# Performance work log

Measured on AMD Instinct MI355X. Metric: run time of the kernel, lower is better.

The kernel has to match this reference:

```python
import jax, jax.numpy as jnp
import numpy as np

B, C, H, W = 8, 2, 512, 512  # features hard-coded to 2 by Conv3x3(2,1)
N_ATTN = 6  # 3 ResidualAttentionUnits x 2 AttentionConv each
HALF = C // 2


def _conv1x1(x, w, b):
    # x: [B,C,H,W], w: [O,C], b: [O]
    return jnp.einsum('bchw,oc->bohw', x, w) + b[None, :, None, None]


def _unfold3(x):
    # x: [B,C,H+2,W+2] -> [B,C,H,W,3,3] (height-window, width-window), matching
    # torch unfold(2,3,1).unfold(3,3,1)
    Hh = x.shape[2] - 2
    Ww = x.shape[3] - 2
    return jnp.stack(
        [jnp.stack([x[:, :, i:i + Hh, j:j + Ww] for j in range(3)], axis=-1)
         for i in range(3)], axis=-2)


def _attn_conv(x, wq, bq, wk, bk, wv, bv, rh, rw):
    # Local 3x3 window self-attention (AttentionConv, groups=1).
    b_, c_, h_, w_ = x.shape
    xp = jnp.pad(x, ((0, 0), (0, 0), (1, 1), (1, 1)))  # zero pad=1
    q = _conv1x1(x, wq, bq)                 # [B,Co,H,W]
    k = _unfold3(_conv1x1(xp, wk, bk))      # [B,Co,H,W,3,3]
    v = _unfold3(_conv1x1(xp, wv, bv))
    co = q.shape[1]
    half = co // 2
    # rh, rw: [half,3]; rel_h broadcast over kh, rel_w over kw
    k = jnp.concatenate([
        k[:, :half] + rh[None, :, None, None, :, None],
        k[:, half:] + rw[None, :, None, None, None, :]], axis=1)
    k = k.reshape(b_, co, h_, w_, 9)
    v = v.reshape(b_, co, h_, w_, 9)
    attn = jax.nn.softmax(q[..., None] * k, axis=-1)  # softmax over 9 window positions
    return jnp.einsum('bchwk,bchwk->bchw', attn, v)


def _rau(x, p, u):
    # ResidualAttentionUnit: relu -> atten1 -> relu -> atten2 -> +x
    wq, bq, wk, bk, wv, bv, rh, rw = p
    i, j = 2 * u, 2 * u + 1
    h = jax.nn.relu(x)
    h = _attn_conv(h, wq[i], bq[i], wk[i], bk[i], wv[i], bv[i], rh[i], rw[i])
    h = jax.nn.relu(h)
    h = _attn_conv(h, wq[j], bq[j], wk[j], bk[j], wv[j], bv[j], rh[j], rw[j])
    return h + x


def _up2_bilinear_ac(x):
    # bilinear, scale_factor=2, align_corners=True
    b_, c_, h_, w_ = x.shape
    ho, wo = 2 * h_, 2 * w_
    ys = jnp.linspace(0.0, h_ - 1.0, ho)
    xs = jnp.linspace(0.0, w_ - 1.0, wo)
    y0 = jnp.floor(ys).astype(jnp.int32)
    x0 = jnp.floor(xs).astype(jnp.int32)
    y1 = jnp.clip(y0 + 1, 0, h_ - 1)
    x1 = jnp.clip(x0 + 1, 0, w_ - 1)
    wy = (ys - y0)[None, None, :, None]
    wx = (xs - x0)[None, None, None, :]
    r0 = x[:, :, y0, :]
    r1 = x[:, :, y1, :]
    v00 = r0[:, :, :, x0]
    v01 = r0[:, :, :, x1]
    v10 = r1[:, :, :, x0]
    v11 = r1[:, :, :, x1]
    return (v00 * (1 - wy) * (1 - wx) + v01 * (1 - wy) * wx
            + v10 * wy * (1 - wx) + v11 * wy * wx)


def _forward(input_1, input_2, wq, bq, wk, bk, wv, bv, rh, rw, conv_w, conv_b):
    p = (wq, bq, wk, bk, wv, bv, rh, rw)
    out = _rau(input_1, p, 0) + _rau(input_2, p, 1)
    out = _rau(out, p, 2)
    xp = jnp.pad(out, ((0, 0), (0, 0), (1, 1), (1, 1)), mode='reflect')
    out = jax.lax.conv_general_dilated(
        xp, conv_w, (1, 1), 'VALID',
        dimension_numbers=('NCHW', 'OIHW', 'NCHW')) + conv_b[None, :, None, None]
    out = jax.nn.sigmoid(out)
    return out, _up2_bilinear_ac(out)


def setup_inputs() -> dict:
    key = jax.random.key(0)
    ks = jax.random.split(key, 12)
    return {
        'input_1': jax.random.normal(ks[0], (B, C, H, W), jnp.float32),
        'input_2': jax.random.normal(ks[1], (B, C, H, W), jnp.float32),
        # stacked params for the 6 AttentionConv modules (all bias=True)
        'wq': jax.random.normal(ks[2], (N_ATTN, C, C), jnp.float32) * 0.5,
        'bq': jax.random.normal(ks[3], (N_ATTN, C), jnp.float32) * 0.1,
        'wk': jax.random.normal(ks[4], (N_ATTN, C, C), jnp.float32) * 0.5,
        'bk': jax.random.normal(ks[5], (N_ATTN, C), jnp.float32) * 0.1,
        'wv': jax.random.normal(ks[6], (N_ATTN, C, C), jnp.float32) * 0.5,
        'bv': jax.random.normal(ks[7], (N_ATTN, C), jnp.float32) * 0.1,
        'rh': jax.random.normal(ks[8], (N_ATTN, HALF, 3), jnp.float32),
        'rw': jax.random.normal(ks[9], (N_ATTN, HALF, 3), jnp.float32),
        # Conv3x3(2,1): reflection-pad + 3x3 conv
        'conv_w': jax.random.normal(ks[10], (1, 2, 3, 3), jnp.float32) * 0.2,
        'conv_b': jax.random.normal(ks[11], (1,), jnp.float32) * 0.1,
    }


def reference(input_1, input_2, wq, bq, wk, bk, wv, bv, rh, rw, conv_w, conv_b):
    return _forward(input_1, input_2, wq, bq, wk, bk, wv, bv, rh, rw, conv_w, conv_b)
```

## Files before the change

kernel.cpp:

```cpp
#include <hip/hip_runtime.h>

#if __has_builtin(__builtin_amdgcn_exp2f)
#define EXP2F(x) __builtin_amdgcn_exp2f(x)
#else
#define EXP2F(x) exp2f(x)
#endif

typedef float v2f __attribute__((ext_vector_type(2)));

constexpr int B = 8, H = 512, W = 512;
constexpr int PLANE = H * W;
constexpr int BSTRIDE = 2 * PLANE;
constexpr int NPIX = B * PLANE;
constexpr int PPITCH = 520;
constexpr int PXOFF  = 4;
constexpr int PPLANE = H * PPITCH;
constexpr int PBUF   = 16 * PPLANE;
constexpr float LOG2E = 1.4426950408889634f;

__device__ __forceinline__ float reluf(float v) { return v > 0.f ? v : 0.f; }
__device__ __forceinline__ float frcp(float v) { return __builtin_amdgcn_rcpf(v); }
__device__ __forceinline__ v2f vfma(v2f a, v2f b, v2f c) { return __builtin_elementwise_fma(a, b, c); }
__device__ __forceinline__ v2f vmax2(v2f a, v2f b) { return __builtin_elementwise_max(a, b); }
__device__ __forceinline__ v2f bc(float x) { v2f r; r.x = x; r.y = x; return r; }

__device__ __forceinline__ unsigned swz8(unsigned bid, unsigned nwg)
{
    return (bid & 7u) * (nwg >> 3) + (bid >> 3);
}

struct AttnW {
    v2f wq0, wq1, bq;
    v2f wk0, wk1;
    v2f biasK[3];
    float rwL[3];
    v2f wv0, wv1, bv;
};

__device__ __forceinline__ AttnW load_w(
    const float* wq, const float* bq, const float* wk, const float* bk,
    const float* wv, const float* bv, const float* rh, const float* rw, int i)
{
    AttnW P;
    P.wq0.x = wq[4*i];   P.wq0.y = wq[4*i+2];
    P.wq1.x = wq[4*i+1]; P.wq1.y = wq[4*i+3];
    P.bq.x  = bq[2*i];   P.bq.y  = bq[2*i+1];
    P.wk0.x = wk[4*i]   * LOG2E; P.wk0.y = wk[4*i+2] * LOG2E;
    P.wk1.x = wk[4*i+1] * LOG2E; P.wk1.y = wk[4*i+3] * LOG2E;
    float bk1L = bk[2*i+1] * LOG2E;
#pragma unroll
    for (int r = 0; r < 3; ++r) {
        P.biasK[r].x = (bk[2*i] + rh[3*i+r]) * LOG2E;
        P.biasK[r].y = bk1L;
    }
#pragma unroll
    for (int d = 0; d < 3; ++d) P.rwL[d] = rw[3*i+d] * LOG2E;
    P.wv0.x = wv[4*i];   P.wv0.y = wv[4*i+2];
    P.wv1.x = wv[4*i+1]; P.wv1.y = wv[4*i+3];
    P.bv.x  = bv[2*i];   P.bv.y  = bv[2*i+1];
    return P;
}

__device__ __forceinline__ void attn_strip(
    const v2f (&t)[3][6], const AttnW& P, v2f (&o)[4])
{
    v2f kk[3][6], vv[3][6];
#pragma unroll
    for (int r = 0; r < 3; ++r)
#pragma unroll
        for (int c = 0; c < 6; ++c) {
            v2f u0 = bc(t[r][c].x), u1 = bc(t[r][c].y);
            kk[r][c] = vfma(P.wk0, u0, vfma(P.wk1, u1, P.biasK[r]));
            vv[r][c] = vfma(P.wv0, u0, vfma(P.wv1, u1, P.bv));
        }
#pragma unroll
    for (int px = 0; px < 4; ++px) {
        v2f q = vfma(P.wq0, bc(t[1][px+1].x), vfma(P.wq1, bc(t[1][px+1].y), P.bq));
        v2f addv[3];
#pragma unroll
        for (int d = 0; d < 3; ++d) { addv[d].x = 0.f; addv[d].y = q.y * P.rwL[d]; }
        v2f s[9];
#pragma unroll
        for (int r = 0; r < 3; ++r)
#pragma unroll
            for (int d = 0; d < 3; ++d)
                s[r*3+d] = vfma(q, kk[r][px+d], addv[d]);
        v2f m = vmax2(vmax2(vmax2(vmax2(s[0], s[1]), vmax2(s[2], s[3])),
                            vmax2(vmax2(s[4], s[5]), vmax2(s[6], s[7]))), s[8]);
        v2f sum = bc(0.f), acc = bc(0.f);
#pragma unroll
        for (int r = 0; r < 3; ++r)
#pragma unroll
            for (int d = 0; d < 3; ++d) {
                v2f dd = s[r*3+d] - m;
                v2f e; e.x = EXP2F(dd.x); e.y = EXP2F(dd.y);
                sum += e;
                acc = vfma(e, vv[r][px+d], acc);
            }
        v2f rs; rs.x = frcp(sum.x); rs.y = frcp(sum.y);
        o[px] = acc * rs;
    }
}

__device__ __forceinline__ void write_pads(float* outp, int b2, int y, int x0)
{
    float4 z = make_float4(0.f, 0.f, 0.f, 0.f);
    if (x0 == 0) {
        int pb = b2 * PPLANE + y * PPITCH;
        *reinterpret_cast<float4*>(outp + pb)          = z;
        *reinterpret_cast<float4*>(outp + pb + PPLANE) = z;
    } else if (x0 == W - 4) {
        int pb = b2 * PPLANE + y * PPITCH + PXOFF + W;
        *reinterpret_cast<float4*>(outp + pb)          = z;
        *reinterpret_cast<float4*>(outp + pb + PPLANE) = z;
    }
}


__device__ __forceinline__ void load_t_unpadded(
    unsigned s, const float* __restrict__ x, v2f (&t)[3][6])
{
    int x0 = (s & 127) * 4;
    int y  = (s >> 7) & 511;
    int b  = s >> 16;

    const float* xb = x + b * BSTRIDE;
    bool rowv[3] = { y > 0, true, y < H - 1 };
    int  yr[3]   = { y > 0 ? y - 1 : 0, y, y < H - 1 ? y + 1 : H - 1 };
    bool lv   = x0 > 0;
    bool rvld = x0 < W - 4;
    int  xl = lv ? x0 - 1 : 0;
    int  xr = rvld ? x0 + 4 : W - 1;

#pragma unroll
    for (int r = 0; r < 3; ++r) {
        const float* p0 = xb + yr[r] * W;
        const float* p1 = p0 + PLANE;
        float4 a0 = *reinterpret_cast<const float4*>(p0 + x0);
        float4 a1 = *reinterpret_cast<const float4*>(p1 + x0);
        float u0[6] = { p0[xl], a0.x, a0.y, a0.z, a0.w, p0[xr] };
        float u1[6] = { p1[xl], a1.x, a1.y, a1.z, a1.w, p1[xr] };
        bool rv_ = rowv[r];
#pragma unroll
        for (int c = 0; c < 6; ++c) {
            bool ok = rv_ && (c > 0 || lv) && (c < 5 || rvld);
            t[r][c].x = ok ? reluf(u0[c]) : 0.f;
            t[r][c].y = ok ? reluf(u1[c]) : 0.f;
        }
    }
}

__device__ __forceinline__ void load_t_padded(
    unsigned s, const float* __restrict__ xp, v2f (&t)[3][6])
{
    int x0 = (s & 127) * 4;
    int y  = (s >> 7) & 511;
    int b  = s >> 16;

    const float* xb0 = xp + (b * 2) * PPLANE + x0 + PXOFF;
#pragma unroll
    for (int r = 0; r < 3; ++r) {
        int gy = y - 1 + r;
        bool ok = (unsigned)gy < (unsigned)H;
        int gyc = ok ? gy : y;
        const float* p0 = xb0 + gyc * PPITCH;
        const float* p1 = p0 + PPLANE;
        float4 a0 = *reinterpret_cast<const float4*>(p0);
        float4 a1 = *reinterpret_cast<const float4*>(p1);
        float e0l = p0[-1], e0r = p0[4];
        float e1l = p1[-1], e1r = p1[4];
        if (ok) {
            t[r][0].x=reluf(e0l);  t[r][0].y=reluf(e1l);
            t[r][1].x=reluf(a0.x); t[r][1].y=reluf(a1.x);
            t[r][2].x=reluf(a0.y); t[r][2].y=reluf(a1.y);
            t[r][3].x=reluf(a0.z); t[r][3].y=reluf(a1.z);
            t[r][4].x=reluf(a0.w); t[r][4].y=reluf(a1.w);
            t[r][5].x=reluf(e0r);  t[r][5].y=reluf(e1r);
        } else {
#pragma unroll
            for (int c = 0; c < 6; ++c) { t[r][c].x = 0.f; t[r][c].y = 0.f; }
        }
    }
}


__global__ __launch_bounds__(256) void attn_in_kernel(
    const float* __restrict__ xA, const float* __restrict__ xB,
    float* outA, float* outB,
    const float* __restrict__ wq, const float* __restrict__ bq,
    const float* __restrict__ wk, const float* __restrict__ bk,
    const float* __restrict__ wv, const float* __restrict__ bv,
    const float* __restrict__ rh, const float* __restrict__ rw,
    int piA, int piB)
{
    unsigned wid = swz8(blockIdx.x, 4096);
    bool second = wid >= 2048;
    AttnW P = load_w(wq, bq, wk, bk, wv, bv, rh, rw, second ? piB : piA);
    unsigned s = (second ? wid - 2048 : wid) * 256u + threadIdx.x;

    v2f t[3][6];
    load_t_unpadded(s, second ? xB : xA, t);
    v2f o[4];
    attn_strip(t, P, o);

    int x0 = (s & 127) * 4;
    int y  = (s >> 7) & 511;
    int b  = s >> 16;
    float* outp = second ? outB : outA;
    int ob = (b * 2) * PPLANE + y * PPITCH + x0 + PXOFF;
    *reinterpret_cast<float4*>(outp + ob)          = make_float4(o[0].x, o[1].x, o[2].x, o[3].x);
    *reinterpret_cast<float4*>(outp + ob + PPLANE) = make_float4(o[0].y, o[1].y, o[2].y, o[3].y);
    write_pads(outp, b * 2, y, x0);
}

__global__ __launch_bounds__(256) void attn_fused23_kernel(
    const float* __restrict__ A, const float* __restrict__ Bb,
    const float* __restrict__ in1, const float* __restrict__ in2,
    float* __restrict__ C,
    const float* __restrict__ wq, const float* __restrict__ bq,
    const float* __restrict__ wk, const float* __restrict__ bk,
    const float* __restrict__ wv, const float* __restrict__ bv,
    const float* __restrict__ rh, const float* __restrict__ rw)
{
    unsigned s = swz8(blockIdx.x, 2048) * 256u + threadIdx.x;
    int x0 = (s & 127) * 4;
    int y  = (s >> 7) & 511;
    int b  = s >> 16;
    int base0 = b * BSTRIDE + y * W + x0;
    int base1 = base0 + PLANE;

    v2f t[3][6];
    v2f o1[4], o2[4];

    {
        AttnW P1 = load_w(wq, bq, wk, bk, wv, bv, rh, rw, 1);
        load_t_padded(s, A, t);
        attn_strip(t, P1, o1);
        float4 ra = *reinterpret_cast<const float4*>(in1 + base0);
        float4 rb = *reinterpret_cast<const float4*>(in1 + base1);
        o1[0].x += ra.x; o1[1].x += ra.y; o1[2].x += ra.z; o1[3].x += ra.w;
        o1[0].y += rb.x; o1[1].y += rb.y; o1[2].y += rb.z; o1[3].y += rb.w;
    }
    {
        AttnW P3 = load_w(wq, bq, wk, bk, wv, bv, rh, rw, 3);
        load_t_padded(s, Bb, t);
        attn_strip(t, P3, o2);
        float4 ra = *reinterpret_cast<const float4*>(in2 + base0);
        float4 rb = *reinterpret_cast<const float4*>(in2 + base1);
        o2[0].x += ra.x + o1[0].x; o2[1].x += ra.y + o1[1].x;
        o2[2].x += ra.z + o1[2].x; o2[3].x += ra.w + o1[3].x;
        o2[0].y += rb.x + o1[0].y; o2[1].y += rb.y + o1[1].y;
        o2[2].y += rb.z + o1[2].y; o2[3].y += rb.w + o1[3].y;
    }

    *reinterpret_cast<float4*>(C + base0) = make_float4(o2[0].x, o2[1].x, o2[2].x, o2[3].x);
    *reinterpret_cast<float4*>(C + base1) = make_float4(o2[0].y, o2[1].y, o2[2].y, o2[3].y);
}

__global__ __launch_bounds__(256) void attn4_kernel(
    const float* __restrict__ C, float* __restrict__ Bb,
    const float* __restrict__ wq, const float* __restrict__ bq,
    const float* __restrict__ wk, const float* __restrict__ bk,
    const float* __restrict__ wv, const float* __restrict__ bv,
    const float* __restrict__ rh, const float* __restrict__ rw)
{
    unsigned s = swz8(blockIdx.x, 2048) * 256u + threadIdx.x;
    AttnW P = load_w(wq, bq, wk, bk, wv, bv, rh, rw, 4);
    v2f t[3][6];
    load_t_unpadded(s, C, t);
    v2f o[4];
    attn_strip(t, P, o);

    int x0 = (s & 127) * 4;
    int y  = (s >> 7) & 511;
    int b  = s >> 16;
    int ob = (b * 2) * PPLANE + y * PPITCH + x0 + PXOFF;
    *reinterpret_cast<float4*>(Bb + ob)          = make_float4(o[0].x, o[1].x, o[2].x, o[3].x);
    *reinterpret_cast<float4*>(Bb + ob + PPLANE) = make_float4(o[0].y, o[1].y, o[2].y, o[3].y);
    write_pads(Bb, b * 2, y, x0);
}

__global__ __launch_bounds__(256) void attn5_kernel(
    const float* __restrict__ Bb, float* __restrict__ C,
    const float* __restrict__ wq, const float* __restrict__ bq,
    const float* __restrict__ wk, const float* __restrict__ bk,
    const float* __restrict__ wv, const float* __restrict__ bv,
    const float* __restrict__ rh, const float* __restrict__ rw)
{
    unsigned s = swz8(blockIdx.x, 2048) * 256u + threadIdx.x;
    AttnW P = load_w(wq, bq, wk, bk, wv, bv, rh, rw, 5);
    v2f t[3][6];
    load_t_padded(s, Bb, t);
    v2f o[4];
    attn_strip(t, P, o);

    int x0 = (s & 127) * 4;
    int y  = (s >> 7) & 511;
    int b  = s >> 16;
    int base0 = b * BSTRIDE + y * W + x0;
    int base1 = base0 + PLANE;
    float4 ra = *reinterpret_cast<const float4*>(C + base0);
    float4 rb = *reinterpret_cast<const float4*>(C + base1);
    o[0].x += ra.x; o[1].x += ra.y; o[2].x += ra.z; o[3].x += ra.w;
    o[0].y += rb.x; o[1].y += rb.y; o[2].y += rb.z; o[3].y += rb.w;
    *reinterpret_cast<float4*>(C + base0) = make_float4(o[0].x, o[1].x, o[2].x, o[3].x);
    *reinterpret_cast<float4*>(C + base1) = make_float4(o[0].y, o[1].y, o[2].y, o[3].y);
}

__global__ __launch_bounds__(256) void conv_sig4_kernel(
    const float* __restrict__ u,
    const float* __restrict__ cw, const float* __restrict__ cb,
    float* __restrict__ o)
{
    unsigned s = swz8(blockIdx.x, 2048) * 256u + threadIdx.x;
    int x0 = (s & 127) * 4;
    int y  = (s >> 7) & 511;
    int b  = s >> 16;

    float w[18];
#pragma unroll
    for (int i = 0; i < 18; ++i) w[i] = cw[i];

    int yy[3];
#pragma unroll
    for (int i = 0; i < 3; ++i) {
        int t = y + i - 1;
        if (t < 0) t = -t;
        if (t > H - 1) t = 2 * (H - 1) - t;
        yy[i] = t;
    }
    int xl = x0 - 1; if (xl < 0) xl = 1;
    int xr = x0 + 4; if (xr > W - 1) xr = 2 * (W - 1) - xr;

    float acc[4] = { cb[0], cb[0], cb[0], cb[0] };
#pragma unroll
    for (int c = 0; c < 2; ++c) {
        const float* up = u + b * BSTRIDE + c * PLANE;
#pragma unroll
        for (int i = 0; i < 3; ++i) {
            const float* row = up + yy[i] * W;
            float4 a = *reinterpret_cast<const float4*>(row + x0);
            float t[6] = { row[xl], a.x, a.y, a.z, a.w, row[xr] };
#pragma unroll
            for (int j = 0; j < 3; ++j) {
                float wc = w[c * 9 + i * 3 + j];
#pragma unroll
                for (int px = 0; px < 4; ++px)
                    acc[px] = fmaf(t[px + j], wc, acc[px]);
            }
        }
    }
    float4 ov;
    ov.x = frcp(1.f + EXP2F(-acc[0] * LOG2E));
    ov.y = frcp(1.f + EXP2F(-acc[1] * LOG2E));
    ov.z = frcp(1.f + EXP2F(-acc[2] * LOG2E));
    ov.w = frcp(1.f + EXP2F(-acc[3] * LOG2E));
    *reinterpret_cast<float4*>(o + b * PLANE + y * W + x0) = ov;
}

__global__ __launch_bounds__(256) void upsample4_kernel(
    const float* __restrict__ o, float* __restrict__ up)
{
    unsigned p = swz8(blockIdx.x, 8192) * 256u + threadIdx.x;
    int b  = p >> 18;
    int y  = (p >> 8) & 1023;
    int x0 = (p & 255) * 4;

    const float scale = 511.0f / 1023.0f;
    float fy = y * scale;
    int y0 = (int)fy;
    float wy = fy - y0;
    int y1 = min(y0 + 1, H - 1);

    const float* ob = o + b * PLANE;
    const float* row0 = ob + y0 * W;
    const float* row1 = ob + y1 * W;

    float4 ov;
    float* ovp = &ov.x;
#pragma unroll
    for (int j = 0; j < 4; ++j) {
        float fx = (x0 + j) * scale;
        int xi = (int)fx;
        float wx = fx - xi;
        int xi1 = min(xi + 1, W - 1);
        float v00 = row0[xi], v01 = row0[xi1];
        float v10 = row1[xi], v11 = row1[xi1];
        float top = fmaf(v01 - v00, wx, v00);
        float bot = fmaf(v11 - v10, wx, v10);
        ovp[j] = fmaf(bot - top, wy, top);
    }
    *reinterpret_cast<float4*>(up + ((long)b << 20) + y * 1024 + x0) = ov;
}

extern "C" void kernel_launch(void* const* d_in, const int* in_sizes, int n_in,
                              void* d_out, int out_size, void* d_ws, size_t ws_size,
                              hipStream_t stream) {
    const float* in1 = (const float*)d_in[0];
    const float* in2 = (const float*)d_in[1];
    const float* wq  = (const float*)d_in[2];
    const float* bq  = (const float*)d_in[3];
    const float* wk  = (const float*)d_in[4];
    const float* bk  = (const float*)d_in[5];
    const float* wv  = (const float*)d_in[6];
    const float* bv  = (const float*)d_in[7];
    const float* rh  = (const float*)d_in[8];
    const float* rw  = (const float*)d_in[9];
    const float* cw  = (const float*)d_in[10];
    const float* cb  = (const float*)d_in[11];

    float* out = (float*)d_out;
    float* A  = out;
    float* Bb = out + PBUF;
    float* C  = (float*)d_ws;
    (void)ws_size; (void)out_size; (void)n_in; (void)in_sizes;

    dim3 blk(256);

    attn_in_kernel<<<4096, blk, 0, stream>>>(in1, in2, A, Bb,
        wq, bq, wk, bk, wv, bv, rh, rw, 0, 2);
    attn_fused23_kernel<<<2048, blk, 0, stream>>>(A, Bb, in1, in2, C,
        wq, bq, wk, bk, wv, bv, rh, rw);
    attn4_kernel<<<2048, blk, 0, stream>>>(C, Bb,
        wq, bq, wk, bk, wv, bv, rh, rw);
    attn5_kernel<<<2048, blk, 0, stream>>>(Bb, C,
        wq, bq, wk, bk, wv, bv, rh, rw);
    conv_sig4_kernel<<<2048, blk, 0, stream>>>(C, cw, cb, out);
    upsample4_kernel<<<8192, blk, 0, stream>>>(out, out + NPIX);
}
```

Baseline: 105.2 us.

## Store intermediate attention activations in fp16 padded buffers

Intermediate tensors A, B and C between the attention stages are now stored as _Float16 in padded-pitch planes instead of fp32. C also moves to the padded layout, so attn4 and attn5 use the padded loader and the conv kernel reads padded fp16. This roughly halves the memory traffic of the intermediate reads and writes in a bandwidth-bound pipeline. It adds fp16 rounding error at every stage boundary, including the residual accumulation in C.

Result: faster. 99.80 us (-5.2%).

```diff
diff --git a/kernel.cpp b/kernel.cpp
--- a/kernel.cpp
+++ b/kernel.cpp
@@ -7,6 +7,8 @@
 #endif
 
 typedef float v2f __attribute__((ext_vector_type(2)));
+typedef _Float16 h2v __attribute__((ext_vector_type(2)));
+typedef _Float16 h4v __attribute__((ext_vector_type(4)));
 
 constexpr int B = 8, H = 512, W = 512;
 constexpr int PLANE = H * W;
@@ -102,20 +104,60 @@
     }
 }
 
-__device__ __forceinline__ void write_pads(float* outp, int b2, int y, int x0)
-{
-    float4 z = make_float4(0.f, 0.f, 0.f, 0.f);
-    if (x0 == 0) {
-        int pb = b2 * PPLANE + y * PPITCH;
-        *reinterpret_cast<float4*>(outp + pb)          = z;
-        *reinterpret_cast<float4*>(outp + pb + PPLANE) = z;
-    } else if (x0 == W - 4) {
-        int pb = b2 * PPLANE + y * PPITCH + PXOFF + W;
-        *reinterpret_cast<float4*>(outp + pb)          = z;
-        *reinterpret_cast<float4*>(outp + pb + PPLANE) = z;
-    }
-}
-
+
+__device__ __forceinline__ void store_padded_h(
+    _Float16* outp, int b2, int y, int x0, const v2f (&o)[4])
+{
+    int ob = b2 * PPLANE + y * PPITCH + x0 + PXOFF;
+    h4v h0, h1;
+    h0.x = (_Float16)o[0].x; h0.y = (_Float16)o[1].x; h0.z = (_Float16)o[2].x; h0.w = (_Float16)o[3].x;
+    h1.x = (_Float16)o[0].y; h1.y = (_Float16)o[1].y; h1.z = (_Float16)o[2].y; h1.w = (_Float16)o[3].y;
+    *reinterpret_cast<h4v*>(outp + ob)          = h0;
+    *reinterpret_cast<h4v*>(outp + ob + PPLANE) = h1;
+    if (x0 == 0 || x0 == W - 4) {
+        h4v z; z.x = z.y = z.z = z.w = (_Float16)0.f;
+        int pb = b2 * PPLANE + y * PPITCH + (x0 == 0 ? 0 : PXOFF + W);
+        *reinterpret_cast<h4v*>(outp + pb)          = z;
+        *reinterpret_cast<h4v*>(outp + pb + PPLANE) = z;
+    }
+}
+
+__device__ __forceinline__ void load_t_padded_h(
+    unsigned s, const _Float16* __restrict__ xp, v2f (&t)[3][6])
+{
+    int x0 = (s & 127) * 4;
+    int y  = (s >> 7) & 511;
+    int b  = s >> 16;
+
+    const _Float16* xb0 = xp + (b * 2) * PPLANE + x0 + PXOFF;
+#pragma unroll
+    for (int r = 0; r < 3; ++r) {
+        int gy = y - 1 + r;
+        bool ok = (unsigned)gy < (unsigned)H;
+        int gyc = ok ? gy : y;
+        const _Float16* p0 = xb0 + gyc * PPITCH;
+        const _Float16* p1 = p0 + PPLANE;
+        h2v a0 = *reinterpret_cast<const h2v*>(p0 - 2);
+        h2v a1 = *reinterpret_cast<const h2v*>(p0);
+        h2v a2 = *reinterpret_cast<const h2v*>(p0 + 2);
+        h2v a3 = *reinterpret_cast<const h2v*>(p0 + 4);
+        h2v c0 = *reinterpret_cast<const h2v*>(p1 - 2);
+        h2v c1 = *reinterpret_cast<const h2v*>(p1);
+        h2v c2 = *reinterpret_cast<const h2v*>(p1 + 2);
+        h2v c3 = *reinterpret_cast<const h2v*>(p1 + 4);
+        if (ok) {
+            t[r][0].x = reluf((float)a0.y); t[r][0].y = reluf((float)c0.y);
+            t[r][1].x = reluf((float)a1.x); t[r][1].y = reluf((float)c1.x);
+            t[r][2].x = reluf((float)a1.y); t[r][2].y = reluf((float)c1.y);
+            t[r][3].x = reluf((float)a2.x); t[r][3].y = reluf((float)c2.x);
+            t[r][4].x = reluf((float)a2.y); t[r][4].y = reluf((float)c2.y);
+            t[r][5].x = reluf((float)a3.x); t[r][5].y = reluf((float)c3.x);
+        } else {
+#pragma unroll
+            for (int c = 0; c < 6; ++c) { t[r][c].x = 0.f; t[r][c].y = 0.f; }
+        }
+    }
+}
 
 __device__ __forceinline__ void load_t_unpadded(
     unsigned s, const float* __restrict__ x, v2f (&t)[3][6])
@@ -150,43 +192,10 @@
     }
 }
 
-__device__ __forceinline__ void load_t_padded(
-    unsigned s, const float* __restrict__ xp, v2f (&t)[3][6])
-{
-    int x0 = (s & 127) * 4;
-    int y  = (s >> 7) & 511;
-    int b  = s >> 16;
-
-    const float* xb0 = xp + (b * 2) * PPLANE + x0 + PXOFF;
-#pragma unroll
-    for (int r = 0; r < 3; ++r) {
-        int gy = y - 1 + r;
-        bool ok = (unsigned)gy < (unsigned)H;
-        int gyc = ok ? gy : y;
-        const float* p0 = xb0 + gyc * PPITCH;
-        const float* p1 = p0 + PPLANE;
-        float4 a0 = *reinterpret_cast<const float4*>(p0);
-        float4 a1 = *reinterpret_cast<const float4*>(p1);
-        float e0l = p0[-1], e0r = p0[4];
-        float e1l = p1[-1], e1r = p1[4];
-        if (ok) {
-            t[r][0].x=reluf(e0l);  t[r][0].y=reluf(e1l);
-            t[r][1].x=reluf(a0.x); t[r][1].y=reluf(a1.x);
-            t[r][2].x=reluf(a0.y); t[r][2].y=reluf(a1.y);
-            t[r][3].x=reluf(a0.z); t[r][3].y=reluf(a1.z);
-            t[r][4].x=reluf(a0.w); t[r][4].y=reluf(a1.w);
-            t[r][5].x=reluf(e0r);  t[r][5].y=reluf(e1r);
-        } else {
-#pragma unroll
-            for (int c = 0; c < 6; ++c) { t[r][c].x = 0.f; t[r][c].y = 0.f; }
-        }
-    }
-}
-
 
 __global__ __launch_bounds__(256) void attn_in_kernel(
     const float* __restrict__ xA, const float* __restrict__ xB,
-    float* outA, float* outB,
+    _Float16* outA, _Float16* outB,
     const float* __restrict__ wq, const float* __restrict__ bq,
     const float* __restrict__ wk, const float* __restrict__ bk,
     const float* __restrict__ wv, const float* __restrict__ bv,
@@ -203,20 +212,13 @@
     v2f o[4];
     attn_strip(t, P, o);
 
-    int x0 = (s & 127) * 4;
-    int y  = (s >> 7) & 511;
-    int b  = s >> 16;
-    float* outp = second ? outB : outA;
-    int ob = (b * 2) * PPLANE + y * PPITCH + x0 + PXOFF;
-    *reinterpret_cast<float4*>(outp + ob)          = make_float4(o[0].x, o[1].x, o[2].x, o[3].x);
-    *reinterpret_cast<float4*>(outp + ob + PPLANE) = make_float4(o[0].y, o[1].y, o[2].y, o[3].y);
-    write_pads(outp, b * 2, y, x0);
+    store_padded_h(second ? outB : outA, (s >> 16) * 2, (s >> 7) & 511, (s & 127) * 4, o);
 }
 
 __global__ __launch_bounds__(256) void attn_fused23_kernel(
-    const float* __restrict__ A, const float* __restrict__ Bb,
+    const _Float16* __restrict__ A, const _Float16* __restrict__ Bb,
     const float* __restrict__ in1, const float* __restrict__ in2,
-    float* __restrict__ C,
+    _Float16* __restrict__ C,
     const float* __restrict__ wq, const float* __restrict__ bq,
     const float* __restrict__ wk, const float* __restrict__ bk,
     const float* __restrict__ wv, const float* __restrict__ bv,
@@ -234,7 +236,7 @@
 
     {
         AttnW P1 = load_w(wq, bq, wk, bk, wv, bv, rh, rw, 1);
-        load_t_padded(s, A, t);
+        load_t_padded_h(s, A, t);
         attn_strip(t, P1, o1);
         float4 ra = *reinterpret_cast<const float4*>(in1 + base0);
         float4 rb = *reinterpret_cast<const float4*>(in1 + base1);
@@ -243,7 +245,7 @@
     }
     {
         AttnW P3 = load_w(wq, bq, wk, bk, wv, bv, rh, rw, 3);
-        load_t_padded(s, Bb, t);
+        load_t_padded_h(s, Bb, t);
         attn_strip(t, P3, o2);
         float4 ra = *reinterpret_cast<const float4*>(in2 + base0);
         float4 rb = *reinterpret_cast<const float4*>(in2 + base1);
@@ -253,12 +255,11 @@
         o2[2].y += rb.z + o1[2].y; o2[3].y += rb.w + o1[3].y;
     }
 
-    *reinterpret_cast<float4*>(C + base0) = make_float4(o2[0].x, o2[1].x, o2[2].x, o2[3].x);
-    *reinterpret_cast<float4*>(C + base1) = make_float4(o2[0].y, o2[1].y, o2[2].y, o2[3].y);
+    store_padded_h(C, b * 2, y, x0, o2);
 }
 
 __global__ __launch_bounds__(256) void attn4_kernel(
-    const float* __restrict__ C, float* __restrict__ Bb,
+    const _Float16* __restrict__ C, _Float16* __restrict__ Bb,
     const float* __restrict__ wq, const float* __restrict__ bq,
     const float* __restrict__ wk, const float* __restrict__ bk,
     const float* __restrict__ wv, const float* __restrict__ bv,
@@ -267,7 +268,23 @@
     unsigned s = swz8(blockIdx.x, 2048) * 256u + threadIdx.x;
     AttnW P = load_w(wq, bq, wk, bk, wv, bv, rh, rw, 4);
     v2f t[3][6];
-    load_t_unpadded(s, C, t);
+    load_t_padded_h(s, C, t);
+    v2f o[4];
+    attn_strip(t, P, o);
+    store_padded_h(Bb, (s >> 16) * 2, (s >> 7) & 511, (s & 127) * 4, o);
+}
+
+__global__ __launch_bounds__(256) void attn5_kernel(
+    const _Float16* __restrict__ Bb, _Float16* __restrict__ C,
+    const float* __restrict__ wq, const float* __restrict__ bq,
+    const float* __restrict__ wk, const float* __restrict__ bk,
+    const float* __restrict__ wv, const float* __restrict__ bv,
+    const float* __restrict__ rh, const float* __restrict__ rw)
+{
+    unsigned s = swz8(blockIdx.x, 2048) * 256u + threadIdx.x;
+    AttnW P = load_w(wq, bq, wk, bk, wv, bv, rh, rw, 5);
+    v2f t[3][6];
+    load_t_padded_h(s, Bb, t);
     v2f o[4];
     attn_strip(t, P, o);
 
@@ -275,40 +292,20 @@
     int y  = (s >> 7) & 511;
     int b  = s >> 16;
     int ob = (b * 2) * PPLANE + y * PPITCH + x0 + PXOFF;
-    *reinterpret_cast<float4*>(Bb + ob)          = make_float4(o[0].x, o[1].x, o[2].x, o[3].x);
-    *reinterpret_cast<float4*>(Bb + ob + PPLANE) = make_float4(o[0].y, o[1].y, o[2].y, o[3].y);
-    write_pads(Bb, b * 2, y, x0);
-}
-
-__global__ __launch_bounds__(256) void attn5_kernel(
-    const float* __restrict__ Bb, float* __restrict__ C,
-    const float* __restrict__ wq, const float* __restrict__ bq,
-    const float* __restrict__ wk, const float* __restrict__ bk,
-    const float* __restrict__ wv, const float* __restrict__ bv,
-    const float* __restrict__ rh, const float* __restrict__ rw)
-{
-    unsigned s = swz8(blockIdx.x, 2048) * 256u + threadIdx.x;
-    AttnW P = load_w(wq, bq, wk, bk, wv, bv, rh, rw, 5);
-    v2f t[3][6];
-    load_t_padded(s, Bb, t);
-    v2f o[4];
-    attn_strip(t, P, o);
-
-    int x0 = (s & 127) * 4;
-    int y  = (s >> 7) & 511;
-    int b  = s >> 16;
-    int base0 = b * BSTRIDE + y * W + x0;
-    int base1 = base0 + PLANE;
-    float4 ra = *reinterpret_cast<const float4*>(C + base0);
-    float4 rb = *reinterpret_cast<const float4*>(C + base1);
-    o[0].x += ra.x; o[1].x += ra.y; o[2].x += ra.z; o[3].x += ra.w;
-    o[0].y += rb.x; o[1].y += rb.y; o[2].y += rb.z; o[3].y += rb.w;
-    *reinterpret_cast<float4*>(C + base0) = make_float4(o[0].x, o[1].x, o[2].x, o[3].x);
-    *reinterpret_cast<float4*>(C + base1) = make_float4(o[0].y, o[1].y, o[2].y, o[3].y);
+    h4v r0 = *reinterpret_cast<const h4v*>(C + ob);
+    h4v r1 = *reinterpret_cast<const h4v*>(C + ob + PPLANE);
+    o[0].x += (float)r0.x; o[1].x += (float)r0.y; o[2].x += (float)r0.z; o[3].x += (float)r0.w;
+    o[0].y += (float)r1.x; o[1].y += (float)r1.y; o[2].y += (float)r1.z; o[3].y += (float)r1.w;
+
+    h4v h0, h1;
+    h0.x = (_Float16)o[0].x; h0.y = (_Float16)o[1].x; h0.z = (_Float16)o[2].x; h0.w = (_Float16)o[3].x;
+    h1.x = (_Float16)o[0].y; h1.y = (_Float16)o[1].y; h1.z = (_Float16)o[2].y; h1.w = (_Float16)o[3].y;
+    *reinterpret_cast<h4v*>(C + ob)          = h0;
+    *reinterpret_cast<h4v*>(C + ob + PPLANE) = h1;
 }
 
 __global__ __launch_bounds__(256) void conv_sig4_kernel(
-    const float* __restrict__ u,
+    const _Float16* __restrict__ u,
     const float* __restrict__ cw, const float* __restrict__ cb,
     float* __restrict__ o)
 {
@@ -335,18 +332,20 @@
     float acc[4] = { cb[0], cb[0], cb[0], cb[0] };
 #pragma unroll
     for (int c = 0; c < 2; ++c) {
-        const float* up = u + b * BSTRIDE + c * PLANE;
+        const _Float16* up = u + (b * 2 + c) * PPLANE + PXOFF;
 #pragma unroll
         for (int i = 0; i < 3; ++i) {
-            const float* row = up + yy[i] * W;
-            float4 a = *reinterpret_cast<const float4*>(row + x0);
-            float t[6] = { row[xl], a.x, a.y, a.z, a.w, row[xr] };
+            const _Float16* row = up + yy[i] * PPITCH;
+            h2v m0 = *reinterpret_cast<const h2v*>(row + x0);
+            h2v m1 = *reinterpret_cast<const h2v*>(row + x0 + 2);
+            float t6[6] = { (float)row[xl], (float)m0.x, (float)m0.y,
+                            (float)m1.x, (float)m1.y, (float)row[xr] };
 #pragma unroll
             for (int j = 0; j < 3; ++j) {
                 float wc = w[c * 9 + i * 3 + j];
 #pragma unroll
                 for (int px = 0; px < 4; ++px)
-                    acc[px] = fmaf(t[px + j], wc, acc[px]);
+                    acc[px] = fmaf(t6[px + j], wc, acc[px]);
             }
         }
     }
@@ -410,9 +409,9 @@
     const float* cb  = (const float*)d_in[11];
 
     float* out = (float*)d_out;
-    float* A  = out;
-    float* Bb = out + PBUF;
-    float* C  = (float*)d_ws;
+    _Float16* A  = (_Float16*)out;
+    _Float16* Bb = (_Float16*)out + PBUF;
+    _Float16* C  = (_Float16*)d_ws;
     (void)ws_size; (void)out_size; (void)n_in; (void)in_sizes;
 
     dim3 blk(256);
```
